# Optimization experiments

Hardware: AMD Instinct MI355X
Metric: run time of the kernel (lower is better)

Reference implementation:

```python
import jax, jax.numpy as jnp
import numpy as np

N_GRID = 64
DX = 1.0 / N_GRID
INV_DX = float(N_GRID)
DT = 5e-4
BOUND = 3
GRAVITY = np.array([0.0, -9.8, 0.0], dtype=np.float32)
P_VOL = (DX * 0.5) ** 3          # particle volume (NCLaw convention)
P_RHO = 1000.0
P_MASS = P_VOL * P_RHO
N_PART = 500000


def setup_inputs() -> dict:
    key = jax.random.key(0)
    k1, k2, k3, k4, k5 = jax.random.split(key, 5)
    # particles inside the domain, away from the boundary
    x = 0.2 + 0.6 * jax.random.uniform(k1, (N_PART, 3), dtype=jnp.float32)
    v = 0.1 * jax.random.normal(k2, (N_PART, 3), dtype=jnp.float32)
    C = 0.1 * jax.random.normal(k3, (N_PART, 3, 3), dtype=jnp.float32)
    F = jnp.eye(3, dtype=jnp.float32)[None] + 0.01 * jax.random.normal(k4, (N_PART, 3, 3), dtype=jnp.float32)
    s = jax.random.normal(k5, (N_PART, 3, 3), dtype=jnp.float32)
    stress = 100.0 * 0.5 * (s + jnp.swapaxes(s, -1, -2))  # symmetric Cauchy stress
    return {"x": x, "v": v, "C": C, "F": F, "stress": stress}


def _mpm_step(x, v, C, F, stress):
    # quadratic B-spline stencil
    base = jnp.floor(x * INV_DX - 0.5).astype(jnp.int32)        # [N,3]
    fx = x * INV_DX - base.astype(x.dtype)                      # [N,3]
    # weights per offset (0,1,2) per axis -> [N,3(off),3(dim)]
    w = jnp.stack([0.5 * (1.5 - fx) ** 2,
                   0.75 - (fx - 1.0) ** 2,
                   0.5 * (fx - 0.5) ** 2], axis=1)
    # MLS-MPM fused stress + APIC affine term
    affine = stress * (-DT * P_VOL * 4.0 * INV_DX * INV_DX) + P_MASS * C  # [N,3,3]

    offs = jnp.stack(jnp.meshgrid(jnp.arange(3), jnp.arange(3), jnp.arange(3),
                                  indexing='ij'), axis=-1).reshape(27, 3)  # [27,3]
    wi = w[:, offs[:, 0], 0] * w[:, offs[:, 1], 1] * w[:, offs[:, 2], 2]   # [N,27]
    dpos = (offs[None, :, :].astype(x.dtype) - fx[:, None, :]) * DX        # [N,27,3] physical
    mom = P_MASS * v[:, None, :] + jnp.einsum('nij,nkj->nki', affine, dpos)  # [N,27,3]

    idx = base[:, None, :] + offs[None, :, :]                               # [N,27,3]
    flat = (idx[..., 0] * N_GRID + idx[..., 1]) * N_GRID + idx[..., 2]      # [N,27]
    flat_r = flat.reshape(-1)
    G = N_GRID ** 3
    grid_mv = jnp.zeros((G, 3), dtype=x.dtype).at[flat_r].add((wi[..., None] * mom).reshape(-1, 3))
    grid_m = jnp.zeros((G,), dtype=x.dtype).at[flat_r].add((wi * P_MASS).reshape(-1))

    has_mass = grid_m > 0.0
    grid_v = jnp.where(has_mass[:, None], grid_mv / jnp.maximum(grid_m, 1e-10)[:, None], 0.0)
    grid_v = jnp.where(has_mass[:, None], grid_v + DT * jnp.asarray(GRAVITY, x.dtype), 0.0)

    # sticky-ish boundary: zero inflow velocity near walls
    gi = jnp.arange(G)
    ijk = jnp.stack([gi // (N_GRID * N_GRID), (gi // N_GRID) % N_GRID, gi % N_GRID], axis=-1)
    low = (ijk < BOUND) & (grid_v < 0.0)
    high = (ijk >= N_GRID - BOUND) & (grid_v > 0.0)
    grid_v = jnp.where(low | high, 0.0, grid_v)

    # G2P gather
    gv = grid_v[flat]                                              # [N,27,3]
    v_next = jnp.einsum('nk,nkd->nd', wi, gv)                      # [N,3]
    C_next = (4.0 * INV_DX * INV_DX) * jnp.einsum('nk,nki,nkj->nij', wi, gv, dpos)
    x_next = x + DT * v_next
    F_next = jnp.einsum('nij,njk->nik', jnp.eye(3, dtype=x.dtype)[None] + DT * C_next, F)
    return x_next, v_next, C_next, F_next


def reference(x, v, C, F, stress):
    return _mpm_step(x, v, C, F, stress)
```

## Files before the change

kernel.cpp:

```cpp
#include <hip/hip_runtime.h>
#include <math.h>

namespace {
constexpr int   NG    = 64;
constexpr int   GC    = NG * NG * NG;
constexpr int   BOUND = 3;
constexpr float DXf    = 1.0f / 64.0f;
constexpr float INV_DX = 64.0f;
constexpr float DTf    = 5e-4f;
constexpr double P_VOL_D = (0.5 / 64.0) * (0.5 / 64.0) * (0.5 / 64.0);
constexpr float P_MASS_F = (float)(P_VOL_D * 1000.0);
constexpr float AFFINE_SCALE = (float)(-5e-4 * P_VOL_D * 4.0 * 64.0 * 64.0);
constexpr float D_INV  = 4.0f * 64.0f * 64.0f;
constexpr float GRAV_Y = -9.8f;

__device__ __forceinline__ void atom_add_f32(float* p, float v) {
    unsafeAtomicAdd(p, v);
}

__device__ __forceinline__ void weights_of(float fx0, float fx1, float fx2, float w[3][3]) {
    w[0][0] = 0.5f*(1.5f-fx0)*(1.5f-fx0); w[0][1] = 0.5f*(1.5f-fx1)*(1.5f-fx1); w[0][2] = 0.5f*(1.5f-fx2)*(1.5f-fx2);
    w[1][0] = 0.75f-(fx0-1.0f)*(fx0-1.0f); w[1][1] = 0.75f-(fx1-1.0f)*(fx1-1.0f); w[1][2] = 0.75f-(fx2-1.0f)*(fx2-1.0f);
    w[2][0] = 0.5f*(fx0-0.5f)*(fx0-0.5f); w[2][1] = 0.5f*(fx1-0.5f)*(fx1-0.5f); w[2][2] = 0.5f*(fx2-0.5f)*(fx2-0.5f);
}

__device__ __forceinline__ float bspline_w(float u) {
    float au = fabsf(u);
    float a  = 1.5f - au;
    float w  = (au < 0.5f) ? (0.75f - u * u) : (0.5f * a * a);
    return (au < 1.5f) ? w : 0.f;
}
}

__global__ __launch_bounds__(256) void count_kernel(const float* __restrict__ x,
                                                    int* __restrict__ cnt, int n)
{
    int p = blockIdx.x * 256 + threadIdx.x;
    if (p >= n) return;
    float u0 = x[3*p] * INV_DX, u1 = x[3*p+1] * INV_DX, u2 = x[3*p+2] * INV_DX;
    int b0 = (int)floorf(u0 - 0.5f), b1 = (int)floorf(u1 - 0.5f), b2 = (int)floorf(u2 - 0.5f);
    if ((unsigned)b0 >= 64u || (unsigned)b1 >= 64u || (unsigned)b2 >= 64u) return;
    atomicAdd(&cnt[((b0 << 6) + b1) * 64 + b2], 1);
}

__global__ __launch_bounds__(256) void scanA(const int* __restrict__ cnt,
                                             int* __restrict__ start,
                                             int* __restrict__ aux)
{
    __shared__ int sh[256];
    int tid = threadIdx.x;
    int i = blockIdx.x * 256 + tid;
    int v = cnt[i];
    sh[tid] = v;
    __syncthreads();
    for (int off = 1; off < 256; off <<= 1) {
        int t = (tid >= off) ? sh[tid - off] : 0;
        __syncthreads();
        sh[tid] += t;
        __syncthreads();
    }
    start[i] = sh[tid] - v;
    if (tid == 255) aux[blockIdx.x] = sh[255];
}

__global__ __launch_bounds__(256) void scanB(int* __restrict__ aux,
                                             int* __restrict__ start)
{
    __shared__ int partial[256];
    int tid = threadIdx.x;
    int local[4];
    int s = 0;
#pragma unroll
    for (int i = 0; i < 4; ++i) { local[i] = s; s += aux[tid * 4 + i]; }
    partial[tid] = s;
    __syncthreads();
    for (int off = 1; off < 256; off <<= 1) {
        int v = (tid >= off) ? partial[tid - off] : 0;
        __syncthreads();
        partial[tid] += v;
        __syncthreads();
    }
    int base = (tid > 0) ? partial[tid - 1] : 0;
#pragma unroll
    for (int i = 0; i < 4; ++i) aux[tid * 4 + i] = base + local[i];
    if (tid == 255) start[GC] = partial[255];
}

__global__ __launch_bounds__(256) void scanC(int* __restrict__ start,
                                             const int* __restrict__ aux,
                                             int* __restrict__ cursor)
{
    int i = blockIdx.x * 256 + threadIdx.x;
    int v = start[i] + aux[blockIdx.x];
    start[i] = v;
    cursor[i] = v;
}

__global__ __launch_bounds__(256) void reorder_kernel(const float* __restrict__ x,
                                                      const float* __restrict__ v,
                                                      const float* __restrict__ C,
                                                      const float* __restrict__ st,
                                                      int* __restrict__ cursor,
                                                      float4* __restrict__ payload, int n)
{
    int p = blockIdx.x * 256 + threadIdx.x;
    if (p >= n) return;

    float u0 = x[3*p] * INV_DX, u1 = x[3*p+1] * INV_DX, u2 = x[3*p+2] * INV_DX;
    int b0 = (int)floorf(u0 - 0.5f), b1 = (int)floorf(u1 - 0.5f), b2 = (int)floorf(u2 - 0.5f);
    if ((unsigned)b0 >= 64u || (unsigned)b1 >= 64u || (unsigned)b2 >= 64u) return;

    float aff[9];
#pragma unroll
    for (int i = 0; i < 9; ++i)
        aff[i] = st[9*p + i] * AFFINE_SCALE + P_MASS_F * C[9*p + i];
    float mv0 = P_MASS_F * v[3*p], mv1 = P_MASS_F * v[3*p+1], mv2 = P_MASS_F * v[3*p+2];

    int pos = atomicAdd(&cursor[((b0 << 6) + b1) * 64 + b2], 1);

    float4* dst = payload + 4 * (size_t)pos;
    dst[0] = make_float4(aff[0], aff[1], aff[2], aff[3]);
    dst[1] = make_float4(aff[4], aff[5], aff[6], aff[7]);
    dst[2] = make_float4(aff[8], mv0, mv1, mv2);
    dst[3] = make_float4(u0, u1, u2, 0.f);
}

__global__ __launch_bounds__(64) void p2g_strip(const float4* __restrict__ payload,
                                                const int* __restrict__ start,
                                                float* __restrict__ grid)
{
    int w   = blockIdx.x;
    int xcd = w & 7, j = w >> 3;
    int cj  = j >> 4, oj = j & 15;
    int r   = cj * 128 + xcd * 16 + oj;

    int row01 = r >> 1;
    int g0 = row01 >> 6, g1 = row01 & 63;
    int tid = threadIdx.x;
    int sl = tid >> 3, q = tid & 7;
    int g2b = ((r & 1) << 5) + sl * 4;
    float fg0 = (float)g0, fg1 = (float)g1, fg2b = (float)g2b;

    float a00=0.f,a01=0.f,a02=0.f,a03=0.f;
    float a10=0.f,a11=0.f,a12=0.f,a13=0.f;
    float a20=0.f,a21=0.f,a22=0.f,a23=0.f;
    float a30=0.f,a31=0.f,a32=0.f,a33=0.f;

    int klo = (g2b >= 2) ? g2b - 2 : 0;
    int khi = (g2b + 3 <= 63) ? g2b + 3 : 63;

#define P2G_CELL(CC, A0, A1, A2, A3)                                         \
    {   float u2  = r3.z - (fg2b + (float)CC);                               \
        float w2  = bspline_w(u2);                                           \
        float wq  = w01 * w2;                                                \
        float dp2 = -u2 * DXf;                                               \
        A0 += wq * (m0 + r0.z * dp2);                                        \
        A1 += wq * (m1 + r1.y * dp2);                                        \
        A2 += wq * (m2 + r2.x * dp2);                                        \
        A3 += wq * P_MASS_F; }

#define P2G_SEG(SS, QOFF, STRIDE)                                            \
    {   int o0 = (SS) / 3, o1 = (SS) % 3;                                    \
        int b0 = g0 - o0, b1 = g1 - o1;                                      \
        if ((unsigned)b0 < 64u && (unsigned)b1 < 64u) {                      \
            int rowp = ((b0 << 6) + b1) << 6;                                \
            int s = start[rowp + klo] + (QOFF);                              \
            int e = start[rowp + khi + 1];                                   \
            float4 c0, c1, c2, c3;                                           \
            if (s < e) {                                                     \
                const float4* rp = payload + 4 * (size_t)s;                  \
                c0 = rp[0]; c1 = rp[1]; c2 = rp[2]; c3 = rp[3];              \
            }                                                                \
            for (int idx = s; idx < e; ) {                                   \
                float4 r0 = c0, r1 = c1, r2 = c2, r3 = c3;                   \
                idx += (STRIDE);                                             \
                if (idx < e) {                                               \
                    const float4* rp = payload + 4 * (size_t)idx;            \
                    c0 = rp[0]; c1 = rp[1]; c2 = rp[2]; c3 = rp[3];          \
                }                                                            \
                float u0  = r3.x - fg0, u1 = r3.y - fg1;                     \
                float w01 = bspline_w(u0) * bspline_w(u1);                   \
                float dp0 = -u0 * DXf, dp1 = -u1 * DXf;                      \
                float m0 = r2.y + r0.x * dp0 + r0.y * dp1;                   \
                float m1 = r2.z + r0.w * dp0 + r1.x * dp1;                   \
                float m2 = r2.w + r1.z * dp0 + r1.w * dp1;                   \
                P2G_CELL(0, a00, a01, a02, a03)                              \
                P2G_CELL(1, a10, a11, a12, a13)                              \
                P2G_CELL(2, a20, a21, a22, a23)                              \
                P2G_CELL(3, a30, a31, a32, a33)                              \
            }                                                                \
        }                                                                    \
    }

    P2G_SEG(q, 0, 1)
    P2G_SEG(8, q, 8)
#undef P2G_SEG
#undef P2G_CELL

#define RED(OFF)                                                             \
    a00 += __shfl_down(a00, OFF); a01 += __shfl_down(a01, OFF);              \
    a02 += __shfl_down(a02, OFF); a03 += __shfl_down(a03, OFF);              \
    a10 += __shfl_down(a10, OFF); a11 += __shfl_down(a11, OFF);              \
    a12 += __shfl_down(a12, OFF); a13 += __shfl_down(a13, OFF);              \
    a20 += __shfl_down(a20, OFF); a21 += __shfl_down(a21, OFF);              \
    a22 += __shfl_down(a22, OFF); a23 += __shfl_down(a23, OFF);              \
    a30 += __shfl_down(a30, OFF); a31 += __shfl_down(a31, OFF);              \
    a32 += __shfl_down(a32, OFF); a33 += __shfl_down(a33, OFF);
    RED(1) RED(2) RED(4)
#undef RED

    if (q == 0) {
#define STORE_CELL(CC, A0, A1, A2, A3)                                       \
    {   int g2 = g2b + CC;                                                   \
        float v0 = 0.f, v1 = 0.f, v2 = 0.f;                                  \
        if (A3 > 0.f) {                                                      \
            float mm = fmaxf(A3, 1e-10f);                                    \
            v0 = A0 / mm;                                                    \
            v1 = A1 / mm + DTf * GRAV_Y;                                     \
            v2 = A2 / mm;                                                    \
        }                                                                    \
        if ((g0 < BOUND && v0 < 0.f) || (g0 >= NG - BOUND && v0 > 0.f)) v0 = 0.f; \
        if ((g1 < BOUND && v1 < 0.f) || (g1 >= NG - BOUND && v1 > 0.f)) v1 = 0.f; \
        if ((g2 < BOUND && v2 < 0.f) || (g2 >= NG - BOUND && v2 > 0.f)) v2 = 0.f; \
        ((float4*)grid)[row01 * 64 + g2] = make_float4(v0, v1, v2, A3); }
        STORE_CELL(0, a00, a01, a02, a03)
        STORE_CELL(1, a10, a11, a12, a13)
        STORE_CELL(2, a20, a21, a22, a23)
        STORE_CELL(3, a30, a31, a32, a33)
#undef STORE_CELL
    }
}

__global__ __launch_bounds__(256) void p2g_naive(const float* __restrict__ x,
                                                 const float* __restrict__ v,
                                                 const float* __restrict__ C,
                                                 const float* __restrict__ st,
                                                 float* __restrict__ grid, int n)
{
    int p = blockIdx.x * 256 + threadIdx.x;
    if (p >= n) return;

    float xp0 = x[3*p], xp1 = x[3*p+1], xp2 = x[3*p+2];
    float u0 = xp0 * INV_DX, u1 = xp1 * INV_DX, u2 = xp2 * INV_DX;
    float b0f = floorf(u0 - 0.5f), b1f = floorf(u1 - 0.5f), b2f = floorf(u2 - 0.5f);
    int base0 = (int)b0f, base1 = (int)b1f, base2 = (int)b2f;
    float fx0 = u0 - b0f, fx1 = u1 - b1f, fx2 = u2 - b2f;

    float w[3][3];
    weights_of(fx0, fx1, fx2, w);

    float aff[3][3];
#pragma unroll
    for (int i = 0; i < 3; ++i)
#pragma unroll
        for (int j = 0; j < 3; ++j)
            aff[i][j] = st[9*p + 3*i + j] * AFFINE_SCALE + P_MASS_F * C[9*p + 3*i + j];

    float mv0 = P_MASS_F * v[3*p], mv1 = P_MASS_F * v[3*p+1], mv2 = P_MASS_F * v[3*p+2];

#pragma unroll
    for (int i = 0; i < 3; ++i) {
        float dp0 = ((float)i - fx0) * DXf;
#pragma unroll
        for (int j = 0; j < 3; ++j) {
            float dp1 = ((float)j - fx1) * DXf;
            float wij = w[i][0] * w[j][1];
            float m0 = mv0 + aff[0][0]*dp0 + aff[0][1]*dp1;
            float m1 = mv1 + aff[1][0]*dp0 + aff[1][1]*dp1;
            float m2 = mv2 + aff[2][0]*dp0 + aff[2][1]*dp1;
            int cellij = ((base0 + i) * NG + (base1 + j)) * NG + base2;
#pragma unroll
            for (int k = 0; k < 3; ++k) {
                float dp2 = ((float)k - fx2) * DXf;
                float wi = wij * w[k][2];
                float* cptr = grid + 4 * (cellij + k);
                atom_add_f32(cptr + 0, wi * (m0 + aff[0][2]*dp2));
                atom_add_f32(cptr + 1, wi * (m1 + aff[1][2]*dp2));
                atom_add_f32(cptr + 2, wi * (m2 + aff[2][2]*dp2));
                atom_add_f32(cptr + 3, wi * P_MASS_F);
            }
        }
    }
}

__global__ __launch_bounds__(256) void grid_kernel(float* __restrict__ grid)
{
    int g = blockIdx.x * 256 + threadIdx.x;
    if (g >= GC) return;
    float4 val = ((const float4*)grid)[g];
    float m = val.w;
    float v0 = 0.f, v1 = 0.f, v2 = 0.f;
    if (m > 0.f) {
        float mm = fmaxf(m, 1e-10f);
        v0 = val.x / mm;
        v1 = val.y / mm + DTf * GRAV_Y;
        v2 = val.z / mm;
    }
    int ci = g >> 12, cj = (g >> 6) & 63, ck = g & 63;
    if ((ci < BOUND && v0 < 0.f) || (ci >= NG - BOUND && v0 > 0.f)) v0 = 0.f;
    if ((cj < BOUND && v1 < 0.f) || (cj >= NG - BOUND && v1 > 0.f)) v1 = 0.f;
    if ((ck < BOUND && v2 < 0.f) || (ck >= NG - BOUND && v2 > 0.f)) v2 = 0.f;
    ((float4*)grid)[g] = make_float4(v0, v1, v2, m);
}

__global__ __launch_bounds__(256) void g2p_kernel(const float* __restrict__ x,
                                                  const float* __restrict__ F,
                                                  const float* __restrict__ grid,
                                                  float* __restrict__ out_x,
                                                  float* __restrict__ out_v,
                                                  float* __restrict__ out_C,
                                                  float* __restrict__ out_F,
                                                  int n)
{
    int p = blockIdx.x * 256 + threadIdx.x;
    if (p >= n) return;

    float xp0 = x[3*p], xp1 = x[3*p+1], xp2 = x[3*p+2];
    float t0 = xp0 * INV_DX, t1 = xp1 * INV_DX, t2 = xp2 * INV_DX;
    float b0 = floorf(t0 - 0.5f), b1 = floorf(t1 - 0.5f), b2 = floorf(t2 - 0.5f);
    int   base0 = (int)b0, base1 = (int)b1, base2 = (int)b2;
    float fx0 = t0 - b0, fx1 = t1 - b1, fx2 = t2 - b2;

    float w[3][3];
    weights_of(fx0, fx1, fx2, w);

    float vn0 = 0.f, vn1 = 0.f, vn2 = 0.f;
    float Cn[3][3] = {};

#pragma unroll
    for (int i = 0; i < 3; ++i) {
        float dp0 = ((float)i - fx0) * DXf;
#pragma unroll
        for (int j = 0; j < 3; ++j) {
            float dp1 = ((float)j - fx1) * DXf;
            float wij = w[i][0] * w[j][1];
            int cellij = ((base0 + i) * NG + (base1 + j)) * NG + base2;
#pragma unroll
            for (int k = 0; k < 3; ++k) {
                float dp2 = ((float)k - fx2) * DXf;
                float wi = wij * w[k][2];
                float4 gv = ((const float4*)grid)[cellij + k];
                vn0 += wi * gv.x; vn1 += wi * gv.y; vn2 += wi * gv.z;
                float wx = wi * gv.x, wy = wi * gv.y, wz = wi * gv.z;
                Cn[0][0] += wx * dp0; Cn[0][1] += wx * dp1; Cn[0][2] += wx * dp2;
                Cn[1][0] += wy * dp0; Cn[1][1] += wy * dp1; Cn[1][2] += wy * dp2;
                Cn[2][0] += wz * dp0; Cn[2][1] += wz * dp1; Cn[2][2] += wz * dp2;
            }
        }
    }

#pragma unroll
    for (int i = 0; i < 3; ++i)
#pragma unroll
        for (int j = 0; j < 3; ++j)
            Cn[i][j] *= D_INV;

    out_x[3*p]   = xp0 + DTf * vn0;
    out_x[3*p+1] = xp1 + DTf * vn1;
    out_x[3*p+2] = xp2 + DTf * vn2;
    out_v[3*p]   = vn0; out_v[3*p+1] = vn1; out_v[3*p+2] = vn2;

    float Fp[3][3];
#pragma unroll
    for (int i = 0; i < 3; ++i)
#pragma unroll
        for (int j = 0; j < 3; ++j)
            Fp[i][j] = F[9*p + 3*i + j];

#pragma unroll
    for (int i = 0; i < 3; ++i) {
#pragma unroll
        for (int k = 0; k < 3; ++k) {
            float acc = Cn[i][0]*Fp[0][k] + Cn[i][1]*Fp[1][k] + Cn[i][2]*Fp[2][k];
            out_F[9*p + 3*i + k] = Fp[i][k] + DTf * acc;
            out_C[9*p + 3*i + k] = Cn[i][k];
        }
    }
}

extern "C" void kernel_launch(void* const* d_in, const int* in_sizes, int n_in,
                              void* d_out, int out_size, void* d_ws, size_t ws_size,
                              hipStream_t stream)
{
    const float* x  = (const float*)d_in[0];
    const float* v  = (const float*)d_in[1];
    const float* C  = (const float*)d_in[2];
    const float* F  = (const float*)d_in[3];
    const float* st = (const float*)d_in[4];
    int n = in_sizes[0] / 3;

    const size_t grid_bytes = (size_t)GC * 4 * sizeof(float);
    const size_t tab_ints   = 3 * (size_t)GC + 1 + 1024;
    const bool   use_tiled  = ws_size >= grid_bytes &&
                              (size_t)out_size >= 22 * (size_t)n + tab_ints;

    float* grid = (float*)d_ws;

    float* out  = (float*)d_out;
    float* out_x = out;
    float* out_v = out + 3 * (size_t)n;
    float* out_C = out + 6 * (size_t)n;
    float* out_F = out + 15 * (size_t)n;
    float4* payload = (float4*)(out + 6 * (size_t)n);
    int* tab    = (int*)(out + 22 * (size_t)n);
    int* cnt    = tab;
    int* tstart = tab + GC;
    int* cursor = tab + 2 * GC + 1;
    int* aux    = tab + 3 * GC + 1;

    int pblocks = (n + 255) / 256;

    if (use_tiled) {
        hipMemsetAsync(cnt, 0, (size_t)GC * sizeof(int), stream);
        count_kernel<<<pblocks, 256, 0, stream>>>(x, cnt, n);
        scanA<<<GC / 256, 256, 0, stream>>>(cnt, tstart, aux);
        scanB<<<1, 256, 0, stream>>>(aux, tstart);
        scanC<<<GC / 256, 256, 0, stream>>>(tstart, aux, cursor);
        reorder_kernel<<<pblocks, 256, 0, stream>>>(x, v, C, st, cursor, payload, n);
        p2g_strip<<<GC / 32, 64, 0, stream>>>(payload, tstart, grid);
    } else {
        hipMemsetAsync(grid, 0, grid_bytes, stream);
        p2g_naive<<<pblocks, 256, 0, stream>>>(x, v, C, st, grid, n);
        grid_kernel<<<GC / 256, 256, 0, stream>>>(grid);
    }

    g2p_kernel<<<pblocks, 256, 0, stream>>>(x, F, grid, out_x, out_v, out_C, out_F, n);
}
```

Before: 338.7 us.

## Split particle payload into SoA float4 streams, fuse scan stages, uniform p2g segments

The particle payload is stored as four separate float4 arrays (SoA) instead of four interleaved float4 per particle, so lanes reading consecutive particles make coalesced 16-byte loads in p2g. The single-block scanB is merged into scanC, with every block redundantly scanning the 1024 block sums in shared memory, which removes one kernel launch. The p2g loop over the nine neighbouring rows now gives all 8 lanes a strided share of every row, where before row-per-lane and strided segments were mixed. This trades some redundant scan work per block for fewer launches and better load balance and coalescing.

```diff
diff --git a/kernel.cpp b/kernel.cpp
--- a/kernel.cpp
+++ b/kernel.cpp
@@ -63,15 +63,17 @@
     if (tid == 255) aux[blockIdx.x] = sh[255];
 }
 
-__global__ __launch_bounds__(256) void scanB(int* __restrict__ aux,
-                                             int* __restrict__ start)
+__global__ __launch_bounds__(256) void scanC(int* __restrict__ start,
+                                             const int* __restrict__ aux,
+                                             int* __restrict__ cursor)
 {
     __shared__ int partial[256];
+    __shared__ int sa[1024];
     int tid = threadIdx.x;
     int local[4];
     int s = 0;
 #pragma unroll
-    for (int i = 0; i < 4; ++i) { local[i] = s; s += aux[tid * 4 + i]; }
+    for (int k = 0; k < 4; ++k) { local[k] = s; s += aux[tid * 4 + k]; }
     partial[tid] = s;
     __syncthreads();
     for (int off = 1; off < 256; off <<= 1) {
@@ -82,18 +84,14 @@
     }
     int base = (tid > 0) ? partial[tid - 1] : 0;
 #pragma unroll
-    for (int i = 0; i < 4; ++i) aux[tid * 4 + i] = base + local[i];
-    if (tid == 255) start[GC] = partial[255];
-}
-
-__global__ __launch_bounds__(256) void scanC(int* __restrict__ start,
-                                             const int* __restrict__ aux,
-                                             int* __restrict__ cursor)
-{
-    int i = blockIdx.x * 256 + threadIdx.x;
-    int v = start[i] + aux[blockIdx.x];
+    for (int k = 0; k < 4; ++k) sa[tid * 4 + k] = base + local[k];
+    __syncthreads();
+    int off0 = sa[blockIdx.x];
+    int i = blockIdx.x * 256 + tid;
+    int v = start[i] + off0;
     start[i] = v;
     cursor[i] = v;
+    if (blockIdx.x == 0 && tid == 0) start[GC] = sa[1023] + aux[1023];
 }
 
 __global__ __launch_bounds__(256) void reorder_kernel(const float* __restrict__ x,
@@ -101,7 +99,10 @@
                                                       const float* __restrict__ C,
                                                       const float* __restrict__ st,
                                                       int* __restrict__ cursor,
-                                                      float4* __restrict__ payload, int n)
+                                                      float4* __restrict__ pay0,
+                                                      float4* __restrict__ pay1,
+                                                      float4* __restrict__ pay2,
+                                                      float4* __restrict__ pay3, int n)
 {
     int p = blockIdx.x * 256 + threadIdx.x;
     if (p >= n) return;
@@ -118,14 +119,16 @@
 
     int pos = atomicAdd(&cursor[((b0 << 6) + b1) * 64 + b2], 1);
 
-    float4* dst = payload + 4 * (size_t)pos;
-    dst[0] = make_float4(aff[0], aff[1], aff[2], aff[3]);
-    dst[1] = make_float4(aff[4], aff[5], aff[6], aff[7]);
-    dst[2] = make_float4(aff[8], mv0, mv1, mv2);
-    dst[3] = make_float4(u0, u1, u2, 0.f);
-}
-
-__global__ __launch_bounds__(64) void p2g_strip(const float4* __restrict__ payload,
+    pay0[pos] = make_float4(aff[0], aff[1], aff[2], aff[3]);
+    pay1[pos] = make_float4(aff[4], aff[5], aff[6], aff[7]);
+    pay2[pos] = make_float4(aff[8], mv0, mv1, mv2);
+    pay3[pos] = make_float4(u0, u1, u2, 0.f);
+}
+
+__global__ __launch_bounds__(64) void p2g_strip(const float4* __restrict__ pay0,
+                                                const float4* __restrict__ pay1,
+                                                const float4* __restrict__ pay2,
+                                                const float4* __restrict__ pay3,
                                                 const int* __restrict__ start,
                                                 float* __restrict__ grid)
 {
@@ -159,42 +162,36 @@
         A2 += wq * (m2 + r2.x * dp2);                                        \
         A3 += wq * P_MASS_F; }
 
-#define P2G_SEG(SS, QOFF, STRIDE)                                            \
-    {   int o0 = (SS) / 3, o1 = (SS) % 3;                                    \
-        int b0 = g0 - o0, b1 = g1 - o1;                                      \
-        if ((unsigned)b0 < 64u && (unsigned)b1 < 64u) {                      \
-            int rowp = ((b0 << 6) + b1) << 6;                                \
-            int s = start[rowp + klo] + (QOFF);                              \
-            int e = start[rowp + khi + 1];                                   \
-            float4 c0, c1, c2, c3;                                           \
-            if (s < e) {                                                     \
-                const float4* rp = payload + 4 * (size_t)s;                  \
-                c0 = rp[0]; c1 = rp[1]; c2 = rp[2]; c3 = rp[3];              \
-            }                                                                \
-            for (int idx = s; idx < e; ) {                                   \
-                float4 r0 = c0, r1 = c1, r2 = c2, r3 = c3;                   \
-                idx += (STRIDE);                                             \
-                if (idx < e) {                                               \
-                    const float4* rp = payload + 4 * (size_t)idx;            \
-                    c0 = rp[0]; c1 = rp[1]; c2 = rp[2]; c3 = rp[3];          \
-                }                                                            \
-                float u0  = r3.x - fg0, u1 = r3.y - fg1;                     \
-                float w01 = bspline_w(u0) * bspline_w(u1);                   \
-                float dp0 = -u0 * DXf, dp1 = -u1 * DXf;                      \
-                float m0 = r2.y + r0.x * dp0 + r0.y * dp1;                   \
-                float m1 = r2.z + r0.w * dp0 + r1.x * dp1;                   \
-                float m2 = r2.w + r1.z * dp0 + r1.w * dp1;                   \
-                P2G_CELL(0, a00, a01, a02, a03)                              \
-                P2G_CELL(1, a10, a11, a12, a13)                              \
-                P2G_CELL(2, a20, a21, a22, a23)                              \
-                P2G_CELL(3, a30, a31, a32, a33)                              \
-            }                                                                \
-        }                                                                    \
-    }
-
-    P2G_SEG(q, 0, 1)
-    P2G_SEG(8, q, 8)
-#undef P2G_SEG
+#pragma unroll
+    for (int o0 = 0; o0 < 3; ++o0) {
+        int b0 = g0 - o0;
+        if ((unsigned)b0 >= 64u) continue;
+#pragma unroll
+        for (int o1 = 0; o1 < 3; ++o1) {
+            int b1 = g1 - o1;
+            if ((unsigned)b1 >= 64u) continue;
+            int rowp = ((b0 << 6) + b1) << 6;
+            int s = start[rowp + klo] + q;
+            int e = start[rowp + khi + 1];
+            float4 c0, c1, c2, c3;
+            if (s < e) { c0 = pay0[s]; c1 = pay1[s]; c2 = pay2[s]; c3 = pay3[s]; }
+            for (int idx = s; idx < e; ) {
+                float4 r0 = c0, r1 = c1, r2 = c2, r3 = c3;
+                idx += 8;
+                if (idx < e) { c0 = pay0[idx]; c1 = pay1[idx]; c2 = pay2[idx]; c3 = pay3[idx]; }
+                float u0  = r3.x - fg0, u1 = r3.y - fg1;
+                float w01 = bspline_w(u0) * bspline_w(u1);
+                float dp0 = -u0 * DXf, dp1 = -u1 * DXf;
+                float m0 = r2.y + r0.x * dp0 + r0.y * dp1;
+                float m1 = r2.z + r0.w * dp0 + r1.x * dp1;
+                float m2 = r2.w + r1.z * dp0 + r1.w * dp1;
+                P2G_CELL(0, a00, a01, a02, a03)
+                P2G_CELL(1, a10, a11, a12, a13)
+                P2G_CELL(2, a20, a21, a22, a23)
+                P2G_CELL(3, a30, a31, a32, a33)
+            }
+        }
+    }
 #undef P2G_CELL
 
 #define RED(OFF)                                                             \
@@ -401,7 +398,10 @@
     float* out_v = out + 3 * (size_t)n;
     float* out_C = out + 6 * (size_t)n;
     float* out_F = out + 15 * (size_t)n;
-    float4* payload = (float4*)(out + 6 * (size_t)n);
+    float4* pay0 = (float4*)(out + 6 * (size_t)n);
+    float4* pay1 = pay0 + (size_t)n;
+    float4* pay2 = pay0 + 2 * (size_t)n;
+    float4* pay3 = pay0 + 3 * (size_t)n;
     int* tab    = (int*)(out + 22 * (size_t)n);
     int* cnt    = tab;
     int* tstart = tab + GC;
@@ -414,10 +414,10 @@
         hipMemsetAsync(cnt, 0, (size_t)GC * sizeof(int), stream);
         count_kernel<<<pblocks, 256, 0, stream>>>(x, cnt, n);
         scanA<<<GC / 256, 256, 0, stream>>>(cnt, tstart, aux);
-        scanB<<<1, 256, 0, stream>>>(aux, tstart);
         scanC<<<GC / 256, 256, 0, stream>>>(tstart, aux, cursor);
-        reorder_kernel<<<pblocks, 256, 0, stream>>>(x, v, C, st, cursor, payload, n);
-        p2g_strip<<<GC / 32, 64, 0, stream>>>(payload, tstart, grid);
+        reorder_kernel<<<pblocks, 256, 0, stream>>>(x, v, C, st, cursor,
+                                                    pay0, pay1, pay2, pay3, n);
+        p2g_strip<<<GC / 32, 64, 0, stream>>>(pay0, pay1, pay2, pay3, tstart, grid);
     } else {
         hipMemsetAsync(grid, 0, grid_bytes, stream);
         p2g_naive<<<pblocks, 256, 0, stream>>>(x, v, C, st, grid, n);
```

Result: faster. 320.2 us (-5.5%).
